# Performance work log

Measured on AMD Instinct MI355X. Metric: run time of the kernel, lower is better.

## Reference

```python
import jax, jax.numpy as jnp
import numpy as np
from jax import lax

N_NODES = 150_000
N_EDGES = 1_500_000
N_GRAPHS = 150          # batch_size(30) * sequence_length(5), hardcoded in forward
BATCH_SIZE = 30
SEQ_LEN = 5
IN_F = 1
HID = 100               # gcn_hidden_size == lstm_hidden_size


def setup_inputs() -> dict:
    key = jax.random.key(0)
    ks = jax.random.split(key, 12)
    x = jax.random.normal(ks[0], (N_NODES, IN_F), dtype=jnp.float32)
    edge_index = jax.random.randint(ks[1], (2, N_EDGES), 0, N_NODES, dtype=jnp.int32)
    # 150 graphs of 1000 nodes each (contiguous, as PyG batching produces)
    batch = jnp.repeat(jnp.arange(N_GRAPHS, dtype=jnp.int32), N_NODES // N_GRAPHS)
    s = 0.1
    params = {
        # GCNConv layer 1: Linear(no bias) weight stored [in, out]; separate bias
        "W1": jax.random.normal(ks[2], (IN_F, HID), jnp.float32) * s,
        "b1": jnp.zeros((HID,), jnp.float32),
        # GCNConv layer 2
        "W2": jax.random.normal(ks[3], (HID, HID), jnp.float32) * s,
        "b2": jnp.zeros((HID,), jnp.float32),
        # LSTM (PyTorch gate order i,f,g,o), weights [4H, in]/[4H, H]
        "W_ih": jax.random.normal(ks[4], (4 * HID, HID), jnp.float32) * s,
        "W_hh": jax.random.normal(ks[5], (4 * HID, HID), jnp.float32) * s,
        "b_ih": jnp.zeros((4 * HID,), jnp.float32),
        "b_hh": jnp.zeros((4 * HID,), jnp.float32),
        # output head Linear(HID, 1)
        "W_out": jax.random.normal(ks[6], (1, HID), jnp.float32) * s,
        "b_out": jnp.zeros((1,), jnp.float32),
    }
    return {"x": x, "edge_index": edge_index, "batch": batch, **params}


def _gcn_conv(x, src, dst, W, b, n_nodes):
    """PyG GCNConv: h = W x; out = D^-1/2 (A+I) D^-1/2 h + b."""
    h = x @ W  # [N, HID]
    deg = jax.ops.segment_sum(jnp.ones_like(dst, dtype=h.dtype), dst, num_segments=n_nodes)
    dinv = lax.rsqrt(deg)  # deg >= 1 thanks to self loops
    norm = dinv[src] * dinv[dst]  # [E+N]
    msg = h[src] * norm[:, None]  # gather + scale (memory-bound hot loop)
    out = jax.ops.segment_sum(msg, dst, num_segments=n_nodes)
    return out + b


def _lstm_last_hidden(xs, W_ih, W_hh, b_ih, b_hh):
    """xs: [B, T, H] -> last hidden state [B, H] (single-layer LSTM)."""
    B = xs.shape[0]
    H = W_hh.shape[1]
    h0 = jnp.zeros((B, H), xs.dtype)
    c0 = jnp.zeros((B, H), xs.dtype)

    def step(carry, xt):
        h, c = carry
        gates = xt @ W_ih.T + h @ W_hh.T + (b_ih + b_hh)
        i, f, g, o = jnp.split(gates, 4, axis=-1)
        c = jax.nn.sigmoid(f) * c + jax.nn.sigmoid(i) * jnp.tanh(g)
        h = jax.nn.sigmoid(o) * jnp.tanh(c)
        return (h, c), None

    (h_last, _), _ = lax.scan(step, (h0, c0), jnp.swapaxes(xs, 0, 1))
    return h_last


def reference(x, edge_index, batch, W1, b1, W2, b2, W_ih, W_hh, b_ih, b_hh, W_out, b_out):
    n_nodes = x.shape[0]
    loops = jnp.arange(n_nodes, dtype=edge_index.dtype)
    src = jnp.concatenate([edge_index[0], loops])
    dst = jnp.concatenate([edge_index[1], loops])

    h = _gcn_conv(x, src, dst, W1, b1, n_nodes)
    h = _gcn_conv(h, src, dst, W2, b2, n_nodes)

    # global mean pool over 150 graphs
    sums = jax.ops.segment_sum(h, batch, num_segments=N_GRAPHS)
    cnts = jax.ops.segment_sum(jnp.ones((n_nodes,), h.dtype), batch, num_segments=N_GRAPHS)
    pooled = sums / jnp.maximum(cnts, 1.0)[:, None]  # [150, HID]

    seq = pooled.reshape(BATCH_SIZE, SEQ_LEN, -1)  # [30, 5, HID]
    h_last = _lstm_last_hidden(seq, W_ih, W_hh, b_ih, b_hh)
    prediction = h_last @ W_out.T + b_out  # [30, 1]
    return prediction
```

## Files before the change

### kernel.cpp

```cpp
#include <hip/hip_runtime.h>
#include <math.h>

#define N_NODES   150000
#define N_EDGES   1500000
#define N_GRAPHS  150
#define HID       100
#define BATCH     30
#define SEQ       5
#define NODES_PER_GRAPH 1000

#define NPB   512
#define NB    293
#define SBLK  128
#define SORT_T 512
#define EPB   11720
#define CAP   5632
#define DLMASK 511

__global__ __launch_bounds__(SORT_T) void k_s1(const int* __restrict__ dst,
                                               int* __restrict__ blockBase) {
    __shared__ int hist[NB];
    int t = threadIdx.x;
    for (int i = t; i < NB; i += SORT_T) hist[i] = 0;
    __syncthreads();
    int base = blockIdx.x * EPB;
    int end  = min(base + EPB, N_EDGES);
    for (int i = base + t * 4; i < end; i += SORT_T * 4) {
        int4 d = *reinterpret_cast<const int4*>(dst + i);
        atomicAdd(&hist[d.x >> 9], 1);
        atomicAdd(&hist[d.y >> 9], 1);
        atomicAdd(&hist[d.z >> 9], 1);
        atomicAdd(&hist[d.w >> 9], 1);
    }
    __syncthreads();
    for (int j = t; j < NB; j += SORT_T)
        blockBase[blockIdx.x * NB + j] = hist[j];
}

__global__ __launch_bounds__(SBLK) void k_colscan(int* __restrict__ blockBase,
                                                  int* __restrict__ bucketCount) {
    __shared__ int v[SBLK];
    int j = blockIdx.x;
    int t = threadIdx.x;
    int val = blockBase[t * NB + j];
    v[t] = val;
    __syncthreads();
    for (int off = 1; off < SBLK; off <<= 1) {
        int w = (t >= off) ? v[t - off] : 0;
        __syncthreads();
        v[t] += w;
        __syncthreads();
    }
    blockBase[t * NB + j] = v[t] - val;
    if (t == SBLK - 1) bucketCount[j] = v[t];
}

__global__ __launch_bounds__(SORT_T) void k_s2(const int* __restrict__ src,
                                               const int* __restrict__ dst,
                                               const int* __restrict__ blockBase,
                                               unsigned int* __restrict__ sorted) {
    __shared__ int cursor[NB];
    __shared__ int baseS[NB];
    int t = threadIdx.x;
    const int* bb = blockBase + blockIdx.x * NB;
    for (int i = t; i < NB; i += SORT_T) {
        cursor[i] = 0;
        baseS[i] = i * CAP + bb[i];
    }
    __syncthreads();
    int base = blockIdx.x * EPB;
    int end  = min(base + EPB, N_EDGES);
    for (int i = base + t * 4; i < end; i += SORT_T * 4) {
        int4 s4 = *reinterpret_cast<const int4*>(src + i);
        int4 d4 = *reinterpret_cast<const int4*>(dst + i);
        int bk[4] = { d4.x >> 9, d4.y >> 9, d4.z >> 9, d4.w >> 9 };
        int sv[4] = { s4.x, s4.y, s4.z, s4.w };
        int dl[4] = { d4.x & DLMASK, d4.y & DLMASK, d4.z & DLMASK, d4.w & DLMASK };
        #pragma unroll
        for (int k = 0; k < 4; ++k) {
            int b = bk[k];
            int idx = atomicAdd(&cursor[b], 1);
            sorted[baseS[b] + idx] = ((unsigned int)sv[k] << 9) | (unsigned int)dl[k];
        }
    }
}

__device__ __forceinline__ void bin2_reduce_store(float2 acc, float2* red2, int t,
                                                  float2* __restrict__ outp) {
    red2[t] = acc;
    __syncthreads();
    for (int s = 128; s > 0; s >>= 1) {
        if (t < s) { red2[t].x += red2[t + s].x; red2[t].y += red2[t + s].y; }
        __syncthreads();
    }
    if (t == 0) *outp = red2[0];
}

__global__ __launch_bounds__(256) void k_accA(const unsigned int* __restrict__ sorted,
                                              const int* __restrict__ bucketCount,
                                              const float* __restrict__ x,
                                              float* __restrict__ pd,
                                              float* __restrict__ px,
                                              float2* __restrict__ pW) {
    __shared__ int degI[2][NPB];
    __shared__ float2 red2[256];
    int b = blockIdx.x;
    int t = threadIdx.x;
    int n0 = b << 9;
    int nn = min(NPB, N_NODES - n0);
    degI[0][t] = 0; degI[0][t + 256] = 0;
    degI[1][t] = 0; degI[1][t + 256] = 0;
    __syncthreads();
    int e0 = b * CAP, e1 = e0 + bucketCount[b];
    int rep = t & 1;
    int nvec = (e1 - e0) >> 2;
    for (int v = t; v < nvec; v += 256) {
        uint4 u4 = *reinterpret_cast<const uint4*>(sorted + e0 + v * 4);
        atomicAdd(&degI[rep][u4.x & DLMASK], 1);
        atomicAdd(&degI[rep][u4.y & DLMASK], 1);
        atomicAdd(&degI[rep][u4.z & DLMASK], 1);
        atomicAdd(&degI[rep][u4.w & DLMASK], 1);
    }
    int tail0 = e0 + (nvec << 2);
    if (tail0 + t < e1) atomicAdd(&degI[rep][sorted[tail0 + t] & DLMASK], 1);
    __syncthreads();
    int g0 = n0 / 1000;
    int thresh = (g0 + 1) * 1000 - n0;
    float2 acc = make_float2(0.f, 0.f);
    #pragma unroll
    for (int h = 0; h < 2; ++h) {
        int slot = t + h * 256;
        if (slot < nn) {
            float dv = 1.0f / sqrtf((float)(1 + degI[0][slot] + degI[1][slot]));
            pd[n0 + slot] = dv;
            px[n0 + slot] = dv * x[n0 + slot];
            float v = dv * dv;
            if (slot < thresh) acc.x += v; else acc.y += v;
        }
    }
    bin2_reduce_store(acc, red2, t, &pW[b]);
}

__global__ __launch_bounds__(256) void k_accB(const unsigned int* __restrict__ sorted,
                                              const int* __restrict__ bucketCount,
                                              const float* __restrict__ pd,
                                              const float* __restrict__ px,
                                              float2* __restrict__ pa2,
                                              float2* __restrict__ pA) {
    __shared__ float t1s[2][NPB];
    __shared__ float2 red2[256];
    int b = blockIdx.x;
    int t = threadIdx.x;
    int n0 = b << 9;
    int nn = min(NPB, N_NODES - n0);
    t1s[0][t] = 0.0f; t1s[0][t + 256] = 0.0f;
    t1s[1][t] = 0.0f; t1s[1][t + 256] = 0.0f;
    __syncthreads();
    int e0 = b * CAP, e1 = e0 + bucketCount[b];
    int rep = t & 1;
    int nvec = (e1 - e0) >> 2;
    for (int v = t; v < nvec; v += 256) {
        uint4 u4 = *reinterpret_cast<const uint4*>(sorted + e0 + v * 4);
        float p0 = px[u4.x >> 9];
        float p1 = px[u4.y >> 9];
        float p2 = px[u4.z >> 9];
        float p3 = px[u4.w >> 9];
        atomicAdd(&t1s[rep][u4.x & DLMASK], p0);
        atomicAdd(&t1s[rep][u4.y & DLMASK], p1);
        atomicAdd(&t1s[rep][u4.z & DLMASK], p2);
        atomicAdd(&t1s[rep][u4.w & DLMASK], p3);
    }
    int tail0 = e0 + (nvec << 2);
    if (tail0 + t < e1) {
        unsigned int u = sorted[tail0 + t];
        atomicAdd(&t1s[rep][u & DLMASK], px[u >> 9]);
    }
    __syncthreads();
    int g0 = n0 / 1000;
    int thresh = (g0 + 1) * 1000 - n0;
    float2 acc = make_float2(0.f, 0.f);
    #pragma unroll
    for (int h = 0; h < 2; ++h) {
        int slot = t + h * 256;
        if (slot < nn) {
            float dv = pd[n0 + slot];
            float T1 = t1s[0][slot] + t1s[1][slot];
            float agg1 = dv * T1 + dv * px[n0 + slot];
            float a1 = dv * agg1;
            pa2[n0 + slot] = make_float2(dv, a1);
            float v = dv * a1;
            if (slot < thresh) acc.x += v; else acc.y += v;
        }
    }
    bin2_reduce_store(acc, red2, t, &pA[b]);
}

__global__ __launch_bounds__(256) void k_accG(const unsigned int* __restrict__ sorted,
                                              const int* __restrict__ bucketCount,
                                              const float* __restrict__ pd,
                                              const float2* __restrict__ pa2,
                                              float4* __restrict__ pG) {
    __shared__ float dvl[NPB];
    __shared__ float4 red4[256];
    int b = blockIdx.x;
    int t = threadIdx.x;
    int n0 = b << 9;
    int nn = min(NPB, N_NODES - n0);
    dvl[t]       = (t < nn)       ? pd[n0 + t]       : 0.0f;
    dvl[t + 256] = (t + 256 < nn) ? pd[n0 + t + 256] : 0.0f;
    __syncthreads();
    int g0 = n0 / 1000;
    int thresh = (g0 + 1) * 1000 - n0;
    float sa0 = 0.f, sa1 = 0.f, sw0 = 0.f, sw1 = 0.f;
    int e0 = b * CAP, e1 = e0 + bucketCount[b];
    auto proc = [&](unsigned int u) {
        int dl = (int)(u & DLMASK);
        float dvd = dvl[dl];
        float2 v = pa2[u >> 9];
        if (dl < thresh) { sw0 += dvd * v.x; sa0 += dvd * v.y; }
        else             { sw1 += dvd * v.x; sa1 += dvd * v.y; }
    };
    int nvec = (e1 - e0) >> 2;
    for (int v = t; v < nvec; v += 256) {
        uint4 u4 = *reinterpret_cast<const uint4*>(sorted + e0 + v * 4);
        proc(u4.x); proc(u4.y); proc(u4.z); proc(u4.w);
    }
    int tail0 = e0 + (nvec << 2);
    if (tail0 + t < e1) proc(sorted[tail0 + t]);
    red4[t] = make_float4(sa0, sa1, sw0, sw1);
    __syncthreads();
    for (int s = 128; s > 0; s >>= 1) {
        if (t < s) {
            red4[t].x += red4[t + s].x; red4[t].y += red4[t + s].y;
            red4[t].z += red4[t + s].z; red4[t].w += red4[t + s].w;
        }
        __syncthreads();
    }
    if (t == 0) pG[b] = red4[0];
}

__global__ __launch_bounds__(512) void k_tail(const float2* __restrict__ pW,
                                              const float2* __restrict__ pA,
                                              const float4* __restrict__ pG,
                                              const float* __restrict__ W1,
                                              const float* __restrict__ b1,
                                              const float* __restrict__ W2,
                                              const float* __restrict__ b2,
                                              const float* __restrict__ W_ih,
                                              const float* __restrict__ W_hh,
                                              const float* __restrict__ b_ih,
                                              const float* __restrict__ b_hh,
                                              const float* __restrict__ W_out,
                                              const float* __restrict__ b_out,
                                              float* __restrict__ outp) {
    int b = blockIdx.x;
    int t = threadIdx.x;
    __shared__ float gA[N_GRAPHS], gW[N_GRAPHS];
    __shared__ float v1[HID], v2[HID];
    __shared__ float xs_l[SEQ][HID];
    __shared__ float Xg_l[SEQ][4 * HID];
    __shared__ float hs[HID], cs[HID], gsb[4 * HID];
    __shared__ float red[512];

    if (t < N_GRAPHS) { gA[t] = 0.0f; gW[t] = 0.0f; }
    __syncthreads();
    for (int j = t; j < NB; j += 512) {
        int n0 = j << 9;
        int g0 = n0 / 1000;
        float2 w2v = pW[j];
        float2 a2v = pA[j];
        float4 g4 = pG[j];
        atomicAdd(&gA[g0], a2v.x + g4.x);
        atomicAdd(&gW[g0], w2v.x + g4.z);
        if (g0 + 1 < N_GRAPHS) {
            atomicAdd(&gA[g0 + 1], a2v.y + g4.y);
            atomicAdd(&gW[g0 + 1], w2v.y + g4.w);
        }
    }
    if (t < HID) {
        float a = 0.0f, c = 0.0f;
        for (int k = 0; k < HID; ++k) {
            float w2 = W2[k * HID + t];
            a += W1[k] * w2;
            c += b1[k] * w2;
        }
        v1[t] = a; v2[t] = c;
    }
    __syncthreads();

    if (t < SEQ * HID) {
        int s = t / HID, j = t - s * HID;
        int g = b * SEQ + s;
        float ma = gA[g] * (1.0f / NODES_PER_GRAPH);
        float mw = gW[g] * (1.0f / NODES_PER_GRAPH);
        xs_l[s][j] = ma * v1[j] + mw * v2[j] + b2[j];
    }
    __syncthreads();

    float wreg[HID];
    if (t < 4 * HID) {
        const float4* wp = reinterpret_cast<const float4*>(W_ih + t * HID);
        #pragma unroll
        for (int q = 0; q < HID / 4; ++q) {
            float4 w4 = wp[q];
            wreg[4*q+0] = w4.x; wreg[4*q+1] = w4.y; wreg[4*q+2] = w4.z; wreg[4*q+3] = w4.w;
        }
        float bias = b_ih[t] + b_hh[t];
        for (int s = 0; s < SEQ; ++s) {
            float acc = bias;
            #pragma unroll
            for (int k = 0; k < HID; ++k)
                acc += xs_l[s][k] * wreg[k];
            Xg_l[s][t] = acc;
        }
        wp = reinterpret_cast<const float4*>(W_hh + t * HID);
        #pragma unroll
        for (int q = 0; q < HID / 4; ++q) {
            float4 w4 = wp[q];
            wreg[4*q+0] = w4.x; wreg[4*q+1] = w4.y; wreg[4*q+2] = w4.z; wreg[4*q+3] = w4.w;
        }
    }
    if (t < HID) { hs[t] = 0.0f; cs[t] = 0.0f; }
    __syncthreads();

    for (int step = 0; step < SEQ; ++step) {
        if (t < 4 * HID) {
            float acc = Xg_l[step][t];
            #pragma unroll
            for (int k = 0; k < HID; ++k)
                acc += hs[k] * wreg[k];
            gsb[t] = acc;
        }
        __syncthreads();
        if (t < HID) {
            float ig = 1.0f / (1.0f + expf(-gsb[t]));
            float fg = 1.0f / (1.0f + expf(-gsb[HID + t]));
            float gg = tanhf(gsb[2 * HID + t]);
            float og = 1.0f / (1.0f + expf(-gsb[3 * HID + t]));
            float c  = fg * cs[t] + ig * gg;
            cs[t] = c;
            hs[t] = og * tanhf(c);
        }
        __syncthreads();
    }

    float v = (t < HID) ? hs[t] * W_out[t] : 0.0f;
    red[t] = v;
    __syncthreads();
    for (int s = 256; s > 0; s >>= 1) {
        if (t < s) red[t] += red[t + s];
        __syncthreads();
    }
    if (t == 0) outp[b] = red[0] + b_out[0];
}

static inline char* align_up(char* p, size_t a) {
    return (char*)(((uintptr_t)p + (a - 1)) & ~(uintptr_t)(a - 1));
}

extern "C" void kernel_launch(void* const* d_in, const int* in_sizes, int n_in,
                              void* d_out, int out_size, void* d_ws, size_t ws_size,
                              hipStream_t stream) {
    const float* x    = (const float*)d_in[0];
    const int*   ei   = (const int*)d_in[1];
    const int*   srcp = ei;
    const int*   dstp = ei + N_EDGES;
    const float* W1   = (const float*)d_in[3];
    const float* b1   = (const float*)d_in[4];
    const float* W2   = (const float*)d_in[5];
    const float* b2   = (const float*)d_in[6];
    const float* W_ih = (const float*)d_in[7];
    const float* W_hh = (const float*)d_in[8];
    const float* b_ih = (const float*)d_in[9];
    const float* b_hh = (const float*)d_in[10];
    const float* W_out= (const float*)d_in[11];
    const float* b_out= (const float*)d_in[12];
    float* out = (float*)d_out;

    char* w = (char*)d_ws;
    int*  bucketCount = (int*)w;             w = align_up(w + NB * sizeof(int), 64);
    int*  blockBase   = (int*)w;             w = align_up(w + (size_t)SBLK * NB * sizeof(int), 64);
    unsigned int* sorted = (unsigned int*)w; w = align_up(w + (size_t)NB * CAP * sizeof(unsigned int), 64);
    float*  pd  = (float*)w;                 w = align_up(w + (size_t)N_NODES * sizeof(float), 64);
    float*  px  = (float*)w;                 w = align_up(w + (size_t)N_NODES * sizeof(float), 64);
    float2* pa2 = (float2*)w;                w = align_up(w + (size_t)N_NODES * sizeof(float2), 64);
    float2* pW  = (float2*)w;                w = align_up(w + NB * sizeof(float2), 64);
    float2* pA  = (float2*)w;                w = align_up(w + NB * sizeof(float2), 64);
    float4* pG  = (float4*)w;                w = align_up(w + NB * sizeof(float4), 64);

    k_s1     <<<SBLK, SORT_T, 0, stream>>>(dstp, blockBase);
    k_colscan<<<NB, SBLK, 0, stream>>>(blockBase, bucketCount);
    k_s2     <<<SBLK, SORT_T, 0, stream>>>(srcp, dstp, blockBase, sorted);
    k_accA   <<<NB, 256, 0, stream>>>(sorted, bucketCount, x, pd, px, pW);
    k_accB   <<<NB, 256, 0, stream>>>(sorted, bucketCount, pd, px, pa2, pA);
    k_accG   <<<NB, 256, 0, stream>>>(sorted, bucketCount, pd, pa2, pG);
    k_tail   <<<BATCH, 512, 0, stream>>>(pW, pA, pG, W1, b1, W2, b2,
                                         W_ih, W_hh, b_ih, b_hh, W_out, b_out, out);
}
```

Before: 82.33 us.

## Remove column-scan kernel by computing bucket offsets and counts inline

Drops the separate k_colscan launch. k_s2 now computes each block's bucket base offsets with a serial prefix over earlier blocks' histograms, and each accumulation kernel recomputes its bucket count with a shared-memory reduction over the 128 block histograms. k_accG also reads dinv from pa2 instead of pd. This saves one kernel launch and its dependency gap, at the cost of redundant histogram reads: up to 127 strided loads per thread in k_s2 and three extra reductions.

```diff
diff --git a/kernel.cpp b/kernel.cpp
--- a/kernel.cpp
+++ b/kernel.cpp
@@ -37,24 +37,6 @@
         blockBase[blockIdx.x * NB + j] = hist[j];
 }
 
-__global__ __launch_bounds__(SBLK) void k_colscan(int* __restrict__ blockBase,
-                                                  int* __restrict__ bucketCount) {
-    __shared__ int v[SBLK];
-    int j = blockIdx.x;
-    int t = threadIdx.x;
-    int val = blockBase[t * NB + j];
-    v[t] = val;
-    __syncthreads();
-    for (int off = 1; off < SBLK; off <<= 1) {
-        int w = (t >= off) ? v[t - off] : 0;
-        __syncthreads();
-        v[t] += w;
-        __syncthreads();
-    }
-    blockBase[t * NB + j] = v[t] - val;
-    if (t == SBLK - 1) bucketCount[j] = v[t];
-}
-
 __global__ __launch_bounds__(SORT_T) void k_s2(const int* __restrict__ src,
                                                const int* __restrict__ dst,
                                                const int* __restrict__ blockBase,
@@ -62,13 +44,16 @@
     __shared__ int cursor[NB];
     __shared__ int baseS[NB];
     int t = threadIdx.x;
-    const int* bb = blockBase + blockIdx.x * NB;
-    for (int i = t; i < NB; i += SORT_T) {
-        cursor[i] = 0;
-        baseS[i] = i * CAP + bb[i];
-    }
-    __syncthreads();
-    int base = blockIdx.x * EPB;
+    int blk = blockIdx.x;
+    if (t < NB) {
+        int s = 0;
+        for (int b2 = 0; b2 < blk; ++b2)
+            s += blockBase[b2 * NB + t];
+        baseS[t] = t * CAP + s;
+        cursor[t] = 0;
+    }
+    __syncthreads();
+    int base = blk * EPB;
     int end  = min(base + EPB, N_EDGES);
     for (int i = base + t * 4; i < end; i += SORT_T * 4) {
         int4 s4 = *reinterpret_cast<const int4*>(src + i);
@@ -85,6 +70,19 @@
     }
 }
 
+__device__ __forceinline__ int bucket_count(const int* __restrict__ blockBase,
+                                            int b, int t, int* redI) {
+    redI[t] = (t < SBLK) ? blockBase[t * NB + b] : 0;
+    __syncthreads();
+    for (int s = 128; s > 0; s >>= 1) {
+        if (t < s) redI[t] += redI[t + s];
+        __syncthreads();
+    }
+    int c = redI[0];
+    __syncthreads();
+    return c;
+}
+
 __device__ __forceinline__ void bin2_reduce_store(float2 acc, float2* red2, int t,
                                                   float2* __restrict__ outp) {
     red2[t] = acc;
@@ -97,12 +95,13 @@
 }
 
 __global__ __launch_bounds__(256) void k_accA(const unsigned int* __restrict__ sorted,
-                                              const int* __restrict__ bucketCount,
+                                              const int* __restrict__ blockBase,
                                               const float* __restrict__ x,
                                               float* __restrict__ pd,
                                               float* __restrict__ px,
                                               float2* __restrict__ pW) {
     __shared__ int degI[2][NPB];
+    __shared__ int redI[256];
     __shared__ float2 red2[256];
     int b = blockIdx.x;
     int t = threadIdx.x;
@@ -110,8 +109,9 @@
     int nn = min(NPB, N_NODES - n0);
     degI[0][t] = 0; degI[0][t + 256] = 0;
     degI[1][t] = 0; degI[1][t + 256] = 0;
-    __syncthreads();
-    int e0 = b * CAP, e1 = e0 + bucketCount[b];
+    int bc = bucket_count(blockBase, b, t, redI);
+    __syncthreads();
+    int e0 = b * CAP, e1 = e0 + bc;
     int rep = t & 1;
     int nvec = (e1 - e0) >> 2;
     for (int v = t; v < nvec; v += 256) {
@@ -142,12 +142,13 @@
 }
 
 __global__ __launch_bounds__(256) void k_accB(const unsigned int* __restrict__ sorted,
-                                              const int* __restrict__ bucketCount,
+                                              const int* __restrict__ blockBase,
                                               const float* __restrict__ pd,
                                               const float* __restrict__ px,
                                               float2* __restrict__ pa2,
                                               float2* __restrict__ pA) {
     __shared__ float t1s[2][NPB];
+    __shared__ int redI[256];
     __shared__ float2 red2[256];
     int b = blockIdx.x;
     int t = threadIdx.x;
@@ -155,8 +156,9 @@
     int nn = min(NPB, N_NODES - n0);
     t1s[0][t] = 0.0f; t1s[0][t + 256] = 0.0f;
     t1s[1][t] = 0.0f; t1s[1][t + 256] = 0.0f;
-    __syncthreads();
-    int e0 = b * CAP, e1 = e0 + bucketCount[b];
+    int bc = bucket_count(blockBase, b, t, redI);
+    __syncthreads();
+    int e0 = b * CAP, e1 = e0 + bc;
     int rep = t & 1;
     int nvec = (e1 - e0) >> 2;
     for (int v = t; v < nvec; v += 256) {
@@ -196,23 +198,24 @@
 }
 
 __global__ __launch_bounds__(256) void k_accG(const unsigned int* __restrict__ sorted,
-                                              const int* __restrict__ bucketCount,
-                                              const float* __restrict__ pd,
+                                              const int* __restrict__ blockBase,
                                               const float2* __restrict__ pa2,
                                               float4* __restrict__ pG) {
     __shared__ float dvl[NPB];
+    __shared__ int redI[256];
     __shared__ float4 red4[256];
     int b = blockIdx.x;
     int t = threadIdx.x;
     int n0 = b << 9;
     int nn = min(NPB, N_NODES - n0);
-    dvl[t]       = (t < nn)       ? pd[n0 + t]       : 0.0f;
-    dvl[t + 256] = (t + 256 < nn) ? pd[n0 + t + 256] : 0.0f;
+    dvl[t]       = (t < nn)       ? pa2[n0 + t].x       : 0.0f;
+    dvl[t + 256] = (t + 256 < nn) ? pa2[n0 + t + 256].x : 0.0f;
+    int bc = bucket_count(blockBase, b, t, redI);
     __syncthreads();
     int g0 = n0 / 1000;
     int thresh = (g0 + 1) * 1000 - n0;
     float sa0 = 0.f, sa1 = 0.f, sw0 = 0.f, sw1 = 0.f;
-    int e0 = b * CAP, e1 = e0 + bucketCount[b];
+    int e0 = b * CAP, e1 = e0 + bc;
     auto proc = [&](unsigned int u) {
         int dl = (int)(u & DLMASK);
         float dvd = dvl[dl];
@@ -378,7 +381,6 @@
     float* out = (float*)d_out;
 
     char* w = (char*)d_ws;
-    int*  bucketCount = (int*)w;             w = align_up(w + NB * sizeof(int), 64);
     int*  blockBase   = (int*)w;             w = align_up(w + (size_t)SBLK * NB * sizeof(int), 64);
     unsigned int* sorted = (unsigned int*)w; w = align_up(w + (size_t)NB * CAP * sizeof(unsigned int), 64);
     float*  pd  = (float*)w;                 w = align_up(w + (size_t)N_NODES * sizeof(float), 64);
@@ -388,12 +390,11 @@
     float2* pA  = (float2*)w;                w = align_up(w + NB * sizeof(float2), 64);
     float4* pG  = (float4*)w;                w = align_up(w + NB * sizeof(float4), 64);
 
-    k_s1     <<<SBLK, SORT_T, 0, stream>>>(dstp, blockBase);
-    k_colscan<<<NB, SBLK, 0, stream>>>(blockBase, bucketCount);
-    k_s2     <<<SBLK, SORT_T, 0, stream>>>(srcp, dstp, blockBase, sorted);
-    k_accA   <<<NB, 256, 0, stream>>>(sorted, bucketCount, x, pd, px, pW);
-    k_accB   <<<NB, 256, 0, stream>>>(sorted, bucketCount, pd, px, pa2, pA);
-    k_accG   <<<NB, 256, 0, stream>>>(sorted, bucketCount, pd, pa2, pG);
-    k_tail   <<<BATCH, 512, 0, stream>>>(pW, pA, pG, W1, b1, W2, b2,
-                                         W_ih, W_hh, b_ih, b_hh, W_out, b_out, out);
-}
+    k_s1  <<<SBLK, SORT_T, 0, stream>>>(dstp, blockBase);
+    k_s2  <<<SBLK, SORT_T, 0, stream>>>(srcp, dstp, blockBase, sorted);
+    k_accA<<<NB, 256, 0, stream>>>(sorted, blockBase, x, pd, px, pW);
+    k_accB<<<NB, 256, 0, stream>>>(sorted, blockBase, pd, px, pa2, pA);
+    k_accG<<<NB, 256, 0, stream>>>(sorted, blockBase, pa2, pG);
+    k_tail<<<BATCH, 512, 0, stream>>>(pW, pA, pG, W1, b1, W2, b2,
+                                      W_ih, W_hh, b_ih, b_hh, W_out, b_out, out);
+}
```

Result: slower. 95.83 us (+16.4%).
